# Kernel optimization log

Measured on AMD Instinct MI355X. Metric: run time of the kernel, lower is better.

Reference implementation:

```python
import jax, jax.numpy as jnp
import numpy as np

B, S, D = 2, 2048, 1024
H = 16
HD = D // H

def setup_inputs() -> dict:
    key = jax.random.key(0)
    ks = jax.random.split(key, 9)
    s = 1.0 / np.sqrt(D)
    return {
        "x": jax.random.normal(ks[0], (B, S, D), dtype=jnp.float32),
        "Wq": jax.random.normal(ks[1], (D, D), dtype=jnp.float32) * s,
        "bq": jnp.zeros((D,), dtype=jnp.float32),
        "Wk": jax.random.normal(ks[2], (D, D), dtype=jnp.float32) * s,
        "bk": jnp.zeros((D,), dtype=jnp.float32),
        "Wv": jax.random.normal(ks[3], (D, D), dtype=jnp.float32) * s,
        "bv": jnp.zeros((D,), dtype=jnp.float32),
        "Wo": jax.random.normal(ks[4], (D, D), dtype=jnp.float32) * s,
        "bo": jnp.zeros((D,), dtype=jnp.float32),
    }

def reference(x, Wq, bq, Wk, bk, Wv, bv, Wo, bo):
    b, s, d = x.shape
    # torch Linear: y = x @ W.T + b
    def proj(W, bias):
        y = jnp.einsum('bsd,ed->bse', x, W) + bias
        return y.reshape(b, s, H, HD).transpose(0, 2, 1, 3)  # [b,h,s,hd]
    Q = proj(Wq, bq)
    K = proj(Wk, bk)
    V = proj(Wv, bv)
    scale = 1.0 / jnp.sqrt(jnp.float32(HD))
    scores = jnp.einsum('bhqd,bhkd->bhqk', Q, K) * scale  # [b,h,s,s]
    attn = jax.nn.softmax(scores, axis=-1)
    out = jnp.einsum('bhqk,bhkd->bhqd', attn, V)  # [b,h,s,hd]
    out = out.transpose(0, 2, 1, 3).reshape(b, s, d)
    return jnp.einsum('bsd,ed->bse', out, Wo) + bo
```

## Files before the change

### kernel.cpp

```cpp
#include <hip/hip_runtime.h>
#include <stdint.h>


typedef __bf16 bf16x8 __attribute__((ext_vector_type(8)));
typedef float  f32x4  __attribute__((ext_vector_type(4)));

#define LOG2E 1.44269504088896f
#define FIXED_MAX_BITS 14.4269504088896f

__device__ __forceinline__ unsigned short f2bf(float f) {
    union { float f; unsigned u; } v; v.f = f;
    unsigned r = v.u + 0x7FFFu + ((v.u >> 16) & 1u);
    return (unsigned short)(r >> 16);
}

__device__ __forceinline__ float exp2_fast(float x) {
#if __has_builtin(__builtin_amdgcn_exp2f)
    return __builtin_amdgcn_exp2f(x);
#else
    return __expf(x * 0.69314718056f);
#endif
}

__device__ __forceinline__ void glds16(const void* g, void* l) {
    __builtin_amdgcn_global_load_lds(
        (__attribute__((address_space(1))) void*)(g),
        (__attribute__((address_space(3))) void*)(l),
        16, 0, 0);
}

__global__ __launch_bounds__(256) void cvt_all(
    const float* __restrict__ x,  const float* __restrict__ Wq,
    const float* __restrict__ Wk, const float* __restrict__ Wv,
    const float* __restrict__ Wo,
    unsigned short* __restrict__ xb,  unsigned short* __restrict__ Wqb,
    unsigned short* __restrict__ Wkb, unsigned short* __restrict__ Wvb,
    unsigned short* __restrict__ Wob)
{
    const int stride = gridDim.x * blockDim.x;
    for (int i = blockIdx.x * blockDim.x + threadIdx.x; i < 2097152; i += stride) {
        const float* src; unsigned short* dst; int j;
        if (i < 1048576) { src = x; dst = xb; j = i; }
        else {
            int t = (i - 1048576) >> 18; j = (i - 1048576) & 262143;
            src = (t == 0) ? Wq : (t == 1) ? Wk : (t == 2) ? Wv : Wo;
            dst = (t == 0) ? Wqb : (t == 1) ? Wkb : (t == 2) ? Wvb : Wob;
        }
        float4 v = ((const float4*)src)[j];
        ushort4 o;
        o.x = f2bf(v.x); o.y = f2bf(v.y); o.z = f2bf(v.z); o.w = f2bf(v.w);
        ((ushort4*)dst)[j] = o;
    }
}

template <int MODE>
__global__ __launch_bounds__(256) void gemm_bt(
    const unsigned short* __restrict__ A,
    const unsigned short* __restrict__ W0,
    const unsigned short* __restrict__ W1,
    const unsigned short* __restrict__ W2,
    const float* __restrict__ b0,
    const float* __restrict__ b1,
    const float* __restrict__ b2,
    unsigned short* __restrict__ outQ,
    unsigned short* __restrict__ outK,
    unsigned short* __restrict__ outV,
    float* __restrict__ outF)
{
    constexpr int BM = (MODE == 0) ? 128 : 64;
    constexpr int FM = BM / 32;
    constexpr int RA = BM / 32;

    __shared__ __attribute__((aligned(16))) unsigned short As[2 * BM * 64];
    __shared__ __attribute__((aligned(16))) unsigned short Bs[2 * 128 * 64];

    const int tid  = threadIdx.x;
    const int lane = tid & 63;
    const int wid  = tid >> 6;
    const int quad = lane >> 4;
    const int l16  = lane & 15;

    const int m0 = blockIdx.x * BM;

    const unsigned short* W;
    const float* bias;
    int proj, n0;
    if (MODE == 0) {
        proj = blockIdx.y >> 3;
        n0   = (blockIdx.y & 7) * 128;
        W    = (proj == 0) ? W0 : (proj == 1) ? W1 : W2;
        bias = (proj == 0) ? b0 : (proj == 1) ? b1 : b2;
    } else {
        proj = 0;
        n0   = blockIdx.y * 128;
        W    = W0;
        bias = b0;
    }

    const int wm = (wid >> 1) * (BM / 2);
    const int wn = (wid & 1) * 64;

    f32x4 acc[FM][4];
#pragma unroll
    for (int i = 0; i < FM; ++i)
#pragma unroll
        for (int j = 0; j < 4; ++j)
            acc[i][j] = (f32x4){0.f, 0.f, 0.f, 0.f};

    char* AsB = (char*)As;
    char* BsB = (char*)Bs;

    auto stageAB = [&](int k0, int buf) {
        char* ldsA = AsB + buf * (BM * 128) + wid * 1024;
        char* ldsB = BsB + buf * 16384 + wid * 1024;
#pragma unroll
        for (int q = 0; q < RA; ++q) {
            int i   = q * 256 + tid;
            int row = i >> 3;
            int sc  = (i & 7) ^ (row & 7);
            glds16(A + (size_t)(m0 + row) * 1024 + k0 + sc * 8, ldsA + q * 4096);
        }
#pragma unroll
        for (int q = 0; q < 4; ++q) {
            int i   = q * 256 + tid;
            int row = i >> 3;
            int sc  = (i & 7) ^ (row & 7);
            glds16(W + (size_t)(n0 + row) * 1024 + k0 + sc * 8, ldsB + q * 4096);
        }
    };

    stageAB(0, 0);
    __syncthreads();

    for (int k0 = 0; k0 < 1024; k0 += 64) {
        const int cur = (k0 >> 6) & 1;
        if (k0 + 64 < 1024) stageAB(k0 + 64, cur ^ 1);

        const char* AsC = AsB + cur * (BM * 128);
        const char* BsC = BsB + cur * 16384;

#pragma unroll
        for (int kh = 0; kh < 2; ++kh) {
            bf16x8 af[FM], bfr[4];
#pragma unroll
            for (int t = 0; t < FM; ++t) {
                int r = wm + t * 16 + l16;
                int c = (kh * 4 + quad) ^ (r & 7);
                af[t] = *(const bf16x8*)(AsC + r * 128 + c * 16);
            }
#pragma unroll
            for (int t = 0; t < 4; ++t) {
                int r = wn + t * 16 + l16;
                int c = (kh * 4 + quad) ^ (r & 7);
                bfr[t] = *(const bf16x8*)(BsC + r * 128 + c * 16);
            }
#pragma unroll
            for (int i = 0; i < FM; ++i)
#pragma unroll
                for (int j = 0; j < 4; ++j)
                    acc[i][j] = __builtin_amdgcn_mfma_f32_16x16x32_bf16(
                        af[i], bfr[j], acc[i][j], 0, 0, 0);
        }
        __syncthreads();
    }

#pragma unroll
    for (int i = 0; i < FM; ++i) {
        const int mrow0 = m0 + wm + i * 16 + quad * 4;
#pragma unroll
        for (int j = 0; j < 4; ++j) {
            const int n  = n0 + wn + j * 16 + l16;
            const float bb = bias[n];
            if (MODE == 1) {
#pragma unroll
                for (int r = 0; r < 4; ++r)
                    outF[(size_t)(mrow0 + r) * 1024 + n] = acc[i][j][r] + bb;
            } else {
                const int h = n >> 6, hd = n & 63;
                if (proj == 2) {
                    const int b = mrow0 >> 11, s = mrow0 & 2047;
                    ushort4 pk;
                    pk.x = f2bf(acc[i][j][0] + bb);
                    pk.y = f2bf(acc[i][j][1] + bb);
                    pk.z = f2bf(acc[i][j][2] + bb);
                    pk.w = f2bf(acc[i][j][3] + bb);
                    *(ushort4*)(outV + ((size_t)((b * 16 + h) * 64 + hd)) * 2048 + s) = pk;
                } else {
                    unsigned short* dst = (proj == 0) ? outQ : outK;
                    const float scl = (proj == 0) ? (0.125f * LOG2E) : 1.0f;
#pragma unroll
                    for (int r = 0; r < 4; ++r) {
                        const int m = mrow0 + r;
                        const int b = m >> 11, s = m & 2047;
                        dst[((size_t)((b * 16 + h) * 2048 + s)) * 64 + hd] =
                            f2bf((acc[i][j][r] + bb) * scl);
                    }
                }
            }
        }
    }
}

__global__ __launch_bounds__(256, 4) void attn_kernel(
    const unsigned short* __restrict__ Qb,
    const unsigned short* __restrict__ Kb,
    const unsigned short* __restrict__ Vtb,
    unsigned short* __restrict__ attnb)
{
    __shared__ __attribute__((aligned(16))) unsigned short Ks[2 * 128 * 64];
    __shared__ __attribute__((aligned(16))) unsigned short Vs[2 * 2 * 64 * 64];

    const int tid  = threadIdx.x;
    const int lane = tid & 63;
    const int wid  = tid >> 6;
    const int quad = lane >> 4;
    const int l16  = lane & 15;
    const int l7   = l16 & 7;

    const int bid  = blockIdx.x + (blockIdx.y << 4);
    const int c8   = bid & 7;
    const int t    = bid >> 3;
    const int qt16 = t & 15;
    const int hgrp = t >> 4;
    const int hb   = c8 + (hgrp << 3);
    const int q0   = qt16 * 128 + wid * 32;
    const int bq   = hb >> 4, hh = hb & 15;

    const unsigned short* Qh  = Qb  + (size_t)hb * 2048 * 64;
    const unsigned short* Kh  = Kb  + (size_t)hb * 2048 * 64;
    const unsigned short* Vth = Vtb + (size_t)hb * 64 * 2048;

    bf16x8 qf[2][2];
#pragma unroll
    for (int qt = 0; qt < 2; ++qt) {
        const unsigned short* qp = Qh + (size_t)(q0 + qt * 16 + l16) * 64 + quad * 8;
        qf[qt][0] = *(const bf16x8*)(qp);
        qf[qt][1] = *(const bf16x8*)(qp + 32);
    }

    f32x4 o[4][2];
#pragma unroll
    for (int ht = 0; ht < 4; ++ht)
#pragma unroll
        for (int qt = 0; qt < 2; ++qt)
            o[ht][qt] = (f32x4){0.f, 0.f, 0.f, 0.f};
    float lsum[2] = {0.f, 0.f};

    char* KsB = (char*)Ks;
    char* VsB = (char*)Vs;

    auto stageKV = [&](int kc, int buf) {
        char* ldsK = KsB + buf * 16384 + wid * 1024;
#pragma unroll
        for (int q = 0; q < 4; ++q) {
            int i   = q * 256 + tid;
            int row = i >> 3;
            int g   = (row & 3) | (((row >> 3) & 1) << 2);
            int ch  = (i & 7) ^ g;
            glds16(Kh + (size_t)(kc + row) * 64 + ch * 8, ldsK + q * 4096);
        }
        char* ldsV = VsB + buf * 16384;
#pragma unroll
        for (int sub = 0; sub < 2; ++sub)
#pragma unroll
            for (int q = 0; q < 2; ++q) {
                int i   = q * 256 + tid;
                int row = i >> 3;
                int ch  = (i & 7) ^ (row & 7);
                glds16(Vth + (size_t)row * 2048 + kc + sub * 64 + ch * 8,
                       ldsV + sub * 8192 + wid * 1024 + q * 4096);
            }
    };

    const int base_row = 8 * (l16 >> 2) + (l16 & 3);
    const int kp0 = ((quad) ^ l7) * 16;
    const int kp1 = ((4 + quad) ^ l7) * 16;
    const int vrow = l16 * 128;

    stageKV(0, 0);
    __syncthreads();

    for (int kc = 0; kc < 2048; kc += 128) {
        const int cur = (kc >> 7) & 1;
        if (kc + 128 < 2048) stageKV(kc + 128, cur ^ 1);

        const char* KsC = KsB + cur * 16384;
        const char* VsC = VsB + cur * 16384;

#pragma unroll
        for (int st32 = 0; st32 < 4; ++st32) {
            const char* krb = KsC + (st32 * 32 + base_row) * 128;
            bf16x8 kf00 = *(const bf16x8*)(krb + kp0);
            bf16x8 kf01 = *(const bf16x8*)(krb + kp1);
            bf16x8 kf10 = *(const bf16x8*)(krb + 512 + kp0);
            bf16x8 kf11 = *(const bf16x8*)(krb + 512 + kp1);

            const f32x4 mi = (f32x4){-FIXED_MAX_BITS, -FIXED_MAX_BITS,
                                     -FIXED_MAX_BITS, -FIXED_MAX_BITS};
            f32x4 s00 = mi, s01 = mi, s10 = mi, s11 = mi;
            s00 = __builtin_amdgcn_mfma_f32_16x16x32_bf16(kf00, qf[0][0], s00, 0, 0, 0);
            s00 = __builtin_amdgcn_mfma_f32_16x16x32_bf16(kf01, qf[0][1], s00, 0, 0, 0);
            s01 = __builtin_amdgcn_mfma_f32_16x16x32_bf16(kf10, qf[0][0], s01, 0, 0, 0);
            s01 = __builtin_amdgcn_mfma_f32_16x16x32_bf16(kf11, qf[0][1], s01, 0, 0, 0);
            s10 = __builtin_amdgcn_mfma_f32_16x16x32_bf16(kf00, qf[1][0], s10, 0, 0, 0);
            s10 = __builtin_amdgcn_mfma_f32_16x16x32_bf16(kf01, qf[1][1], s10, 0, 0, 0);
            s11 = __builtin_amdgcn_mfma_f32_16x16x32_bf16(kf10, qf[1][0], s11, 0, 0, 0);
            s11 = __builtin_amdgcn_mfma_f32_16x16x32_bf16(kf11, qf[1][1], s11, 0, 0, 0);

            bf16x8 p8[2];
#pragma unroll
            for (int qt = 0; qt < 2; ++qt) {
                const f32x4 sA = qt ? s10 : s00;
                const f32x4 sB = qt ? s11 : s01;
                float e0 = exp2_fast(sA[0]), e1 = exp2_fast(sA[1]);
                float e2 = exp2_fast(sA[2]), e3 = exp2_fast(sA[3]);
                float e4 = exp2_fast(sB[0]), e5 = exp2_fast(sB[1]);
                float e6 = exp2_fast(sB[2]), e7 = exp2_fast(sB[3]);
                lsum[qt] += ((e0 + e1) + (e2 + e3)) + ((e4 + e5) + (e6 + e7));
                bf16x8 p;
                p[0] = (__bf16)e0; p[1] = (__bf16)e1;
                p[2] = (__bf16)e2; p[3] = (__bf16)e3;
                p[4] = (__bf16)e4; p[5] = (__bf16)e5;
                p[6] = (__bf16)e6; p[7] = (__bf16)e7;
                p8[qt] = p;
            }

            const int voff = (st32 >> 1) * 8192 + vrow
                           + ((((st32 & 1) * 4 + quad) ^ l7) * 16);
#pragma unroll
            for (int ht = 0; ht < 4; ++ht) {
                const bf16x8 vf = *(const bf16x8*)(VsC + voff + ht * 2048);
                o[ht][0] = __builtin_amdgcn_mfma_f32_16x16x32_bf16(vf, p8[0], o[ht][0], 0, 0, 0);
                o[ht][1] = __builtin_amdgcn_mfma_f32_16x16x32_bf16(vf, p8[1], o[ht][1], 0, 0, 0);
            }
        }
        __syncthreads();
    }

    float rl[2];
#pragma unroll
    for (int qt = 0; qt < 2; ++qt) {
        float s = lsum[qt];
        s += __shfl_xor(s, 16);
        s += __shfl_xor(s, 32);
        rl[qt] = 1.0f / s;
    }

#pragma unroll
    for (int qt = 0; qt < 2; ++qt) {
        const size_t row = (size_t)(bq * 2048 + q0 + qt * 16 + l16);
        const float r = rl[qt];
#pragma unroll
        for (int ht = 0; ht < 4; ++ht) {
            ushort4 pk;
            pk.x = f2bf(o[ht][qt][0] * r);
            pk.y = f2bf(o[ht][qt][1] * r);
            pk.z = f2bf(o[ht][qt][2] * r);
            pk.w = f2bf(o[ht][qt][3] * r);
            *(ushort4*)(attnb + row * 1024 + hh * 64 + ht * 16 + quad * 4) = pk;
        }
    }
}

extern "C" void kernel_launch(void* const* d_in, const int* in_sizes, int n_in,
                              void* d_out, int out_size, void* d_ws, size_t ws_size,
                              hipStream_t stream) {
    (void)in_sizes; (void)n_in; (void)out_size; (void)ws_size;

    const float* x  = (const float*)d_in[0];
    const float* Wq = (const float*)d_in[1];
    const float* bq = (const float*)d_in[2];
    const float* Wk = (const float*)d_in[3];
    const float* bk = (const float*)d_in[4];
    const float* Wv = (const float*)d_in[5];
    const float* bv = (const float*)d_in[6];
    const float* Wo = (const float*)d_in[7];
    const float* bo = (const float*)d_in[8];

    char* ws = (char*)d_ws;
    const size_t MB = 1024 * 1024;
    unsigned short* xb    = (unsigned short*)(ws + 0);
    unsigned short* Wqb   = (unsigned short*)(ws + 8  * MB);
    unsigned short* Wkb   = (unsigned short*)(ws + 10 * MB);
    unsigned short* Wvb   = (unsigned short*)(ws + 12 * MB);
    unsigned short* Wob   = (unsigned short*)(ws + 14 * MB);
    unsigned short* Qb    = (unsigned short*)(ws + 16 * MB);
    unsigned short* Kb    = (unsigned short*)(ws + 24 * MB);
    unsigned short* Vtb   = (unsigned short*)(ws + 32 * MB);
    unsigned short* attnb = (unsigned short*)(ws + 40 * MB);

    cvt_all<<<dim3(1024), dim3(256), 0, stream>>>(
        x, Wq, Wk, Wv, Wo, xb, Wqb, Wkb, Wvb, Wob);

    gemm_bt<0><<<dim3(32, 24), dim3(256), 0, stream>>>(
        xb, Wqb, Wkb, Wvb, bq, bk, bv, Qb, Kb, Vtb, nullptr);

    attn_kernel<<<dim3(16, 32), dim3(256), 0, stream>>>(Qb, Kb, Vtb, attnb);

    gemm_bt<1><<<dim3(64, 8), dim3(256), 0, stream>>>(
        attnb, Wob, nullptr, nullptr, bo, nullptr, nullptr,
        nullptr, nullptr, nullptr, (float*)d_out);
}
```

Baseline: 191.6 us.

## Split attention key range across two wave groups per block and merge in LDS

Doubles the attention block to 512 threads, with two groups of four waves each processing half of the key sequence (split-K flash attention inside a block). Each group double-buffers its own 64-key K/V tiles in a separate region of 64KB LDS. At the end the partial outputs and row sums are reduced through LDS. This is meant to raise parallelism and latency hiding per query tile and halve each wave's serial loop length. The cost is double the Q register load, a final LDS reduction with extra syncs, and lower occupancy from the larger LDS footprint.

```diff
diff --git a/kernel.cpp b/kernel.cpp
--- a/kernel.cpp
+++ b/kernel.cpp
@@ -201,18 +201,20 @@
     }
 }
 
-__global__ __launch_bounds__(256, 4) void attn_kernel(
+__global__ __launch_bounds__(512) void attn_kernel(
     const unsigned short* __restrict__ Qb,
     const unsigned short* __restrict__ Kb,
     const unsigned short* __restrict__ Vtb,
     unsigned short* __restrict__ attnb)
 {
-    __shared__ __attribute__((aligned(16))) unsigned short Ks[2 * 128 * 64];
-    __shared__ __attribute__((aligned(16))) unsigned short Vs[2 * 2 * 64 * 64];
+    __shared__ __attribute__((aligned(16))) char SMEM[65536];
 
     const int tid  = threadIdx.x;
     const int lane = tid & 63;
     const int wid  = tid >> 6;
+    const int grp  = wid >> 2;
+    const int qwid = wid & 3;
+    const int gtid = tid & 255;
     const int quad = lane >> 4;
     const int l16  = lane & 15;
     const int l7   = l16 & 7;
@@ -220,10 +222,9 @@
     const int bid  = blockIdx.x + (blockIdx.y << 4);
     const int c8   = bid & 7;
     const int t    = bid >> 3;
+    const int hb   = c8 + ((t >> 4) << 3);
     const int qt16 = t & 15;
-    const int hgrp = t >> 4;
-    const int hb   = c8 + (hgrp << 3);
-    const int q0   = qt16 * 128 + wid * 32;
+    const int q0   = qt16 * 128 + qwid * 32;
     const int bq   = hb >> 4, hh = hb & 15;
 
     const unsigned short* Qh  = Qb  + (size_t)hb * 2048 * 64;
@@ -246,30 +247,28 @@
             o[ht][qt] = (f32x4){0.f, 0.f, 0.f, 0.f};
     float lsum[2] = {0.f, 0.f};
 
-    char* KsB = (char*)Ks;
-    char* VsB = (char*)Vs;
+    char* base = SMEM + grp * 32768;
+    char* KsB  = base;
+    char* VsB  = base + 16384;
 
     auto stageKV = [&](int kc, int buf) {
-        char* ldsK = KsB + buf * 16384 + wid * 1024;
-#pragma unroll
-        for (int q = 0; q < 4; ++q) {
-            int i   = q * 256 + tid;
+        char* ldsK = KsB + buf * 8192 + qwid * 1024;
+#pragma unroll
+        for (int q = 0; q < 2; ++q) {
+            int i   = q * 256 + gtid;
             int row = i >> 3;
             int g   = (row & 3) | (((row >> 3) & 1) << 2);
             int ch  = (i & 7) ^ g;
             glds16(Kh + (size_t)(kc + row) * 64 + ch * 8, ldsK + q * 4096);
         }
-        char* ldsV = VsB + buf * 16384;
-#pragma unroll
-        for (int sub = 0; sub < 2; ++sub)
-#pragma unroll
-            for (int q = 0; q < 2; ++q) {
-                int i   = q * 256 + tid;
-                int row = i >> 3;
-                int ch  = (i & 7) ^ (row & 7);
-                glds16(Vth + (size_t)row * 2048 + kc + sub * 64 + ch * 8,
-                       ldsV + sub * 8192 + wid * 1024 + q * 4096);
-            }
+        char* ldsV = VsB + buf * 8192 + qwid * 1024;
+#pragma unroll
+        for (int q = 0; q < 2; ++q) {
+            int i   = q * 256 + gtid;
+            int row = i >> 3;
+            int ch  = (i & 7) ^ (row & 7);
+            glds16(Vth + (size_t)row * 2048 + kc + ch * 8, ldsV + q * 4096);
+        }
     };
 
     const int base_row = 8 * (l16 >> 2) + (l16 & 3);
@@ -277,18 +276,19 @@
     const int kp1 = ((4 + quad) ^ l7) * 16;
     const int vrow = l16 * 128;
 
-    stageKV(0, 0);
+    const int kc0 = grp * 1024;
+    stageKV(kc0, 0);
     __syncthreads();
 
-    for (int kc = 0; kc < 2048; kc += 128) {
-        const int cur = (kc >> 7) & 1;
-        if (kc + 128 < 2048) stageKV(kc + 128, cur ^ 1);
-
-        const char* KsC = KsB + cur * 16384;
-        const char* VsC = VsB + cur * 16384;
-
-#pragma unroll
-        for (int st32 = 0; st32 < 4; ++st32) {
+    for (int kc = kc0; kc < kc0 + 1024; kc += 64) {
+        const int cur = (kc >> 6) & 1;
+        if (kc + 64 < kc0 + 1024) stageKV(kc + 64, cur ^ 1);
+
+        const char* KsC = KsB + cur * 8192;
+        const char* VsC = VsB + cur * 8192;
+
+#pragma unroll
+        for (int st32 = 0; st32 < 2; ++st32) {
             const char* krb = KsC + (st32 * 32 + base_row) * 128;
             bf16x8 kf00 = *(const bf16x8*)(krb + kp0);
             bf16x8 kf01 = *(const bf16x8*)(krb + kp1);
@@ -325,8 +325,7 @@
                 p8[qt] = p;
             }
 
-            const int voff = (st32 >> 1) * 8192 + vrow
-                           + ((((st32 & 1) * 4 + quad) ^ l7) * 16);
+            const int voff = vrow + (((st32 * 4 + quad) ^ l7) * 16);
 #pragma unroll
             for (int ht = 0; ht < 4; ++ht) {
                 const bf16x8 vf = *(const bf16x8*)(VsC + voff + ht * 2048);
@@ -337,27 +336,48 @@
         __syncthreads();
     }
 
-    float rl[2];
+    float lt[2];
 #pragma unroll
     for (int qt = 0; qt < 2; ++qt) {
         float s = lsum[qt];
         s += __shfl_xor(s, 16);
         s += __shfl_xor(s, 32);
-        rl[qt] = 1.0f / s;
-    }
-
-#pragma unroll
-    for (int qt = 0; qt < 2; ++qt) {
-        const size_t row = (size_t)(bq * 2048 + q0 + qt * 16 + l16);
-        const float r = rl[qt];
-#pragma unroll
-        for (int ht = 0; ht < 4; ++ht) {
-            ushort4 pk;
-            pk.x = f2bf(o[ht][qt][0] * r);
-            pk.y = f2bf(o[ht][qt][1] * r);
-            pk.z = f2bf(o[ht][qt][2] * r);
-            pk.w = f2bf(o[ht][qt][3] * r);
-            *(ushort4*)(attnb + row * 1024 + hh * 64 + ht * 16 + quad * 4) = pk;
+        lt[qt] = s;
+    }
+
+    float* Osc = (float*)SMEM;
+    float* Lsc = (float*)(SMEM + 128 * 65 * 4);
+
+    if (grp == 1) {
+#pragma unroll
+        for (int qt = 0; qt < 2; ++qt) {
+            const int ql = qwid * 32 + qt * 16 + l16;
+#pragma unroll
+            for (int ht = 0; ht < 4; ++ht) {
+#pragma unroll
+                for (int r = 0; r < 4; ++r)
+                    Osc[ql * 65 + ht * 16 + quad * 4 + r] = o[ht][qt][r];
+            }
+            if (quad == 0) Lsc[ql] = lt[qt];
+        }
+    }
+    __syncthreads();
+    if (grp == 0) {
+#pragma unroll
+        for (int qt = 0; qt < 2; ++qt) {
+            const int ql = qwid * 32 + qt * 16 + l16;
+            const float rl = 1.0f / (lt[qt] + Lsc[ql]);
+            const size_t row = (size_t)(bq * 2048 + q0 + qt * 16 + l16);
+#pragma unroll
+            for (int ht = 0; ht < 4; ++ht) {
+                const float* op = &Osc[ql * 65 + ht * 16 + quad * 4];
+                ushort4 pk;
+                pk.x = f2bf((o[ht][qt][0] + op[0]) * rl);
+                pk.y = f2bf((o[ht][qt][1] + op[1]) * rl);
+                pk.z = f2bf((o[ht][qt][2] + op[2]) * rl);
+                pk.w = f2bf((o[ht][qt][3] + op[3]) * rl);
+                *(ushort4*)(attnb + row * 1024 + hh * 64 + ht * 16 + quad * 4) = pk;
+            }
         }
     }
 }
@@ -395,7 +415,7 @@
     gemm_bt<0><<<dim3(32, 24), dim3(256), 0, stream>>>(
         xb, Wqb, Wkb, Wvb, bq, bk, bv, Qb, Kb, Vtb, nullptr);
 
-    attn_kernel<<<dim3(16, 32), dim3(256), 0, stream>>>(Qb, Kb, Vtb, attnb);
+    attn_kernel<<<dim3(16, 32), dim3(512), 0, stream>>>(Qb, Kb, Vtb, attnb);
 
     gemm_bt<1><<<dim3(64, 8), dim3(256), 0, stream>>>(
         attnb, Wob, nullptr, nullptr, bo, nullptr, nullptr,
```

New measurement: 182.5 us. -4.7%, faster.
